# Optimization experiments

Measured on AMD Instinct MI355X. Metric: run time of the kernel, lower is better.

## Reference

```python
import jax, jax.numpy as jnp
import numpy as np

H = 16          # num_heads
R = 4           # query compression ratio
WIN = 128       # sliding window size
NEG = -1e9      # finite mask value (safe softmax grads)


def setup_inputs() -> dict:
    key = jax.random.key(0)
    k0, k1, k2, k3, k4 = jax.random.split(key, 5)
    B, S, D = 4, 4096, 2048
    inputs = jax.random.normal(k0, (B, S, D), jnp.float32)
    attention_mask = jnp.ones((B, S), jnp.int32)
    s = 0.02
    Wq = jax.random.normal(k1, (D, D), jnp.float32) * s
    Wk = jax.random.normal(k2, (D, D), jnp.float32) * s
    Wv = jax.random.normal(k3, (D, D), jnp.float32) * s
    Wo = jax.random.normal(k4, (D, D), jnp.float32) * s
    return {"inputs": inputs, "attention_mask": attention_mask,
            "Wq": Wq, "Wk": Wk, "Wv": Wv, "Wo": Wo}


def _forward(inputs, attention_mask, Wq, Wk, Wv, Wo):
    B, S, D = inputs.shape
    dh = D // H
    scale = 1.0 / np.sqrt(dh).astype(np.float32)
    Cs = (S + R - 1) // R            # compressed query length (S % R == 0 here)
    win = min(WIN, S)
    ws = max(0, S - win)             # window start

    # Q projection -> [B,H,S,dh] -> compress groups of R by mean -> [B,H,Cs,dh]
    q = jnp.einsum('bsd,od->bso', inputs, Wq)
    q = q.reshape(B, S, H, dh).transpose(0, 2, 1, 3)
    qc = q.reshape(B, H, Cs, R, dh).mean(axis=3)

    # K/V only over the recent window
    wx = inputs[:, ws:ws + win, :]
    k = jnp.einsum('bsd,od->bso', wx, Wk).reshape(B, win, H, dh).transpose(0, 2, 1, 3)
    v = jnp.einsum('bsd,od->bso', wx, Wv).reshape(B, win, H, dh).transpose(0, 2, 1, 3)

    scores = jnp.einsum('bhqd,bhkd->bhqk', qc, k) * scale

    # causal mask: each compressed query sits at position (i+1)*R-1
    qpos = (jnp.arange(Cs) + 1) * R - 1                     # [Cs]
    wpos = ws + jnp.arange(win)
    causal = wpos[None, :] <= qpos[:, None]
    qbw = qpos < ws                                         # queries fully before window
    causal = causal.at[:, 0].set(causal[:, 0] | qbw)
    pad_ok = (attention_mask[:, ws:ws + win] != 0)
    full = causal[None, None, :, :] & pad_ok[:, None, None, :]

    scores = jnp.where(full, scores, NEG)
    weights = jax.nn.softmax(scores, axis=-1)
    out = jnp.einsum('bhqk,bhkd->bhqd', weights, v)         # [B,H,Cs,dh]
    out = out.transpose(0, 2, 1, 3).reshape(B, Cs, D)
    out = jnp.einsum('bsd,od->bso', out, Wo)

    if Cs != S:  # linear interpolation back to seq_len (align_corners=False)
        out = jax.image.resize(out, (B, S, D), method='linear')
    return out


def reference(inputs, attention_mask, Wq, Wk, Wv, Wo):
    return _forward(inputs, attention_mask, Wq, Wk, Wv, Wo)
```

## Files before the change

### kernel.cpp

```cpp
#include <hip/hip_runtime.h>
#include <hip/hip_bf16.h>


typedef __attribute__((ext_vector_type(8))) short short8;
typedef __attribute__((ext_vector_type(4))) float f32x4;

#define QP_SLICE  (128 * 2048)
#define KV_SLICE  (512 * 2048)
#define YO_STRIDE (132 * 2048)

__device__ __forceinline__ unsigned short f2bf(float f){
  unsigned int x = __float_as_uint(f);
  return (unsigned short)((x + 0x7fffu + ((x >> 16) & 1u)) >> 16);
}
__device__ __forceinline__ float bf2f(unsigned short u){
  return __uint_as_float(((unsigned int)u) << 16);
}
__device__ __forceinline__ float bflo(unsigned int u){ return __uint_as_float(u << 16); }
__device__ __forceinline__ float bfhi(unsigned int u){ return __uint_as_float(u & 0xffff0000u); }
__device__ __forceinline__ unsigned int pk2(float lo, float hi){
  return ((unsigned int)f2bf(hi) << 16) | (unsigned int)f2bf(lo);
}
__device__ __forceinline__ short8 cvt8(float4 x, float4 y){
  union { unsigned int u[4]; short8 s; } r;
  r.u[0] = pk2(x.x, x.y); r.u[1] = pk2(x.z, x.w);
  r.u[2] = pk2(y.x, y.y); r.u[3] = pk2(y.z, y.w);
  return r.s;
}

__global__ __launch_bounds__(256) void prep_kernel(
    const float* __restrict__ inp,
    const float* __restrict__ Wq, const float* __restrict__ Wk,
    const float* __restrict__ Wv, const float* __restrict__ Wo,
    unsigned short* __restrict__ Wb,
    unsigned short* __restrict__ Awx, unsigned short* __restrict__ Aq)
{
  const int bx = blockIdx.x;
  if (bx < 8192){
    const int idx = bx * 256 + threadIdx.x;
    const int w = idx >> 19;
    const int sub = idx & 524287;
    const float* src = (w == 0) ? Wq : (w == 1) ? Wk : (w == 2) ? Wv : Wo;
    const float* p = src + (size_t)sub * 8;
    *(short8*)&Wb[(size_t)w * 4194304 + (size_t)sub * 8] =
        cvt8(*(const float4*)p, *(const float4*)(p + 4));
  } else if (bx < 8704){
    const int idx = (bx - 8192) * 256 + threadIdx.x;
    const int b = idx >> 15;
    const int j = (idx >> 8) & 127;
    const int d8 = (idx & 255) * 8;
    const float* p = inp + ((size_t)b * 4096 + 3968 + j) * 2048 + d8;
    *(short8*)&Awx[((size_t)b * 128 + j) * 2048 + d8] =
        cvt8(*(const float4*)p, *(const float4*)(p + 4));
  } else {
    const int idx = (bx - 8704) * 256 + threadIdx.x;
    const int b = idx >> 13;
    const int c = (idx >> 8) & 31;
    const int d8 = (idx & 255) * 8;
    const float* p = inp + ((size_t)b * 4096 + 3968 + 4 * c) * 2048 + d8;
    float4 x0 = *(const float4*)(p);
    float4 x1 = *(const float4*)(p + 2048);
    float4 x2 = *(const float4*)(p + 4096);
    float4 x3 = *(const float4*)(p + 6144);
    float4 y0 = *(const float4*)(p + 4);
    float4 y1 = *(const float4*)(p + 2052);
    float4 y2 = *(const float4*)(p + 4100);
    float4 y3 = *(const float4*)(p + 6148);
    float4 xm, ym;
    xm.x = 0.25f * (x0.x + x1.x + x2.x + x3.x);
    xm.y = 0.25f * (x0.y + x1.y + x2.y + x3.y);
    xm.z = 0.25f * (x0.z + x1.z + x2.z + x3.z);
    xm.w = 0.25f * (x0.w + x1.w + x2.w + x3.w);
    ym.x = 0.25f * (y0.x + y1.x + y2.x + y3.x);
    ym.y = 0.25f * (y0.y + y1.y + y2.y + y3.y);
    ym.z = 0.25f * (y0.z + y1.z + y2.z + y3.z);
    ym.w = 0.25f * (y0.w + y1.w + y2.w + y3.w);
    *(short8*)&Aq[((size_t)b * 32 + c) * 2048 + d8] = cvt8(xm, ym);
  }
}

__device__ __forceinline__ void stage_tile(
    const unsigned short* __restrict__ A, const unsigned short* __restrict__ W,
    int row0, int n0, int kt,
    unsigned short* As, unsigned short* Bs, int wid, int lane)
{
  const int r = lane >> 3, u = (lane & 7) * 8;
  #pragma unroll
  for (int i = 0; i < 4; ++i){
    const int c = wid * 4 + i;
    __builtin_amdgcn_global_load_lds(
        (const __attribute__((address_space(1))) void*)(A + (size_t)(row0 + c * 8 + r) * 2048 + kt + u),
        (__attribute__((address_space(3))) void*)(As + c * 512),
        16, 0, 0);
    __builtin_amdgcn_global_load_lds(
        (const __attribute__((address_space(1))) void*)(W + (size_t)(n0 + c * 8 + r) * 2048 + kt + u),
        (__attribute__((address_space(3))) void*)(Bs + c * 512),
        16, 0, 0);
  }
}

template<bool OUT_BF16>
__device__ __forceinline__ void gemm_body(
    const unsigned short* __restrict__ A, const unsigned short* __restrict__ W,
    unsigned short* __restrict__ Cb, float* __restrict__ Cf,
    int M, int row0, int n0, int kbase, int nsteps,
    unsigned short* L)
{
  const int tid  = threadIdx.x;
  const int lane = tid & 63;
  const int wid  = tid >> 6;
  const int wr = wid >> 1, wc = wid & 1;

  f32x4 acc[4][4] = {};

  stage_tile(A, W, row0, n0, kbase, L, L + 8192, wid, lane);
  int cur = 0;

  for (int t = 0; t < nsteps; ++t){
    __syncthreads();
    const int nxt = cur ^ 1;
    if (t + 1 < nsteps)
      stage_tile(A, W, row0, n0, kbase + (t + 1) * 64,
                 L + nxt * 16384, L + nxt * 16384 + 8192, wid, lane);
    const unsigned short* As = L + cur * 16384;
    const unsigned short* Bs = As + 8192;
    #pragma unroll
    for (int ks = 0; ks < 2; ++ks){
      short8 av[4], bv[4];
      #pragma unroll
      for (int f = 0; f < 4; ++f)
        av[f] = *(const short8*)&As[(wr * 64 + f * 16 + (lane & 15)) * 64 + ks * 32 + (lane >> 4) * 8];
      #pragma unroll
      for (int n = 0; n < 4; ++n)
        bv[n] = *(const short8*)&Bs[(wc * 64 + n * 16 + (lane & 15)) * 64 + ks * 32 + (lane >> 4) * 8];
      #pragma unroll
      for (int f = 0; f < 4; ++f)
        #pragma unroll
        for (int n = 0; n < 4; ++n)
          acc[f][n] = __builtin_amdgcn_mfma_f32_16x16x32_bf16(av[f], bv[n], acc[f][n], 0, 0, 0);
    }
    cur = nxt;
  }

  #pragma unroll
  for (int f = 0; f < 4; ++f){
    #pragma unroll
    for (int n = 0; n < 4; ++n){
      const int col = n0 + wc * 64 + n * 16 + (lane & 15);
      #pragma unroll
      for (int r = 0; r < 4; ++r){
        const int row = row0 + wr * 64 + f * 16 + (lane >> 4) * 4 + r;
        if (row < M){
          if (OUT_BF16) Cb[(size_t)row * 2048 + col] = f2bf(acc[f][n][r]);
          else          Cf[(size_t)row * 2048 + col] = acc[f][n][r];
        }
      }
    }
  }
}

__global__ __launch_bounds__(256, 2) void qkv_kernel(
    const unsigned short* __restrict__ Aq, const unsigned short* __restrict__ Awx,
    const unsigned short* __restrict__ Wb,
    unsigned short* __restrict__ Qp, unsigned short* __restrict__ Kp,
    unsigned short* __restrict__ Vp)
{
  __shared__ __align__(16) unsigned short L[4 * 16384 / 2];
  const int nt = blockIdx.x, gy = blockIdx.y;
  if (gy < 4){
    gemm_body<true>(Aq, Wb, Qp + gy * QP_SLICE, nullptr,
                    128, 0, nt * 128, gy * 512, 8, L);
  } else if (gy < 20){
    const int idx = gy - 4, mt = idx >> 2, ksp = idx & 3;
    gemm_body<true>(Awx, Wb + 4194304, Kp + ksp * KV_SLICE, nullptr,
                    512, mt * 128, nt * 128, ksp * 512, 8, L);
  } else {
    const int idx = gy - 20, mt = idx >> 2, ksp = idx & 3;
    gemm_body<true>(Awx, Wb + 8388608, Vp + ksp * KV_SLICE, nullptr,
                    512, mt * 128, nt * 128, ksp * 512, 8, L);
  }
}

__global__ __launch_bounds__(256, 2) void o_kernel(
    const unsigned short* __restrict__ Ao, const unsigned short* __restrict__ Wb,
    float* __restrict__ Yop)
{
  __shared__ __align__(16) unsigned short L[32768];
  gemm_body<false>(Ao, Wb + 12582912, nullptr, Yop + (size_t)blockIdx.z * YO_STRIDE,
                   132, blockIdx.y * 128, blockIdx.x * 128, blockIdx.z * 512, 8, L);
}

__global__ __launch_bounds__(256) void attn_kernel(
    const unsigned short* __restrict__ Qp, const unsigned short* __restrict__ Kp,
    const unsigned short* __restrict__ Vp, const int* __restrict__ amask,
    unsigned short* __restrict__ Ao)
{
  const int b = blockIdx.x >> 4;
  const int h = blockIdx.x & 15;
  __shared__ float Qs[32][129];
  __shared__ unsigned int Ks[128][65];
  __shared__ unsigned int Vs[128][65];
  __shared__ float Wt[32][132];
  __shared__ float msk[128];
  const int tid = threadIdx.x;

  for (int i = tid; i < 32 * 128; i += 256){
    int cq = i >> 7, d = i & 127;
    size_t off = (size_t)(b * 32 + cq) * 2048 + h * 128 + d;
    Qs[cq][d] = bf2f(Qp[off]) + bf2f(Qp[off + QP_SLICE]) +
                bf2f(Qp[off + 2 * QP_SLICE]) + bf2f(Qp[off + 3 * QP_SLICE]);
  }
  for (int i = tid; i < 128 * 64; i += 256){
    int j = i >> 6, du = i & 63;
    size_t off = (size_t)(b * 128 + j) * 2048 + h * 128 + du * 2;
    unsigned int k0 = *(const unsigned int*)(Kp + off);
    unsigned int k1 = *(const unsigned int*)(Kp + off + KV_SLICE);
    unsigned int k2 = *(const unsigned int*)(Kp + off + 2 * KV_SLICE);
    unsigned int k3 = *(const unsigned int*)(Kp + off + 3 * KV_SLICE);
    unsigned int v0 = *(const unsigned int*)(Vp + off);
    unsigned int v1 = *(const unsigned int*)(Vp + off + KV_SLICE);
    unsigned int v2 = *(const unsigned int*)(Vp + off + 2 * KV_SLICE);
    unsigned int v3 = *(const unsigned int*)(Vp + off + 3 * KV_SLICE);
    Ks[j][du] = pk2(bflo(k0) + bflo(k1) + bflo(k2) + bflo(k3),
                    bfhi(k0) + bfhi(k1) + bfhi(k2) + bfhi(k3));
    Vs[j][du] = pk2(bflo(v0) + bflo(v1) + bflo(v2) + bflo(v3),
                    bfhi(v0) + bfhi(v1) + bfhi(v2) + bfhi(v3));
  }
  if (tid < 128){
    msk[tid] = (amask[b * 4096 + 3968 + tid] != 0) ? 1.f : 0.f;
    size_t off = (size_t)(b * 128) * 2048 + h * 128 + tid;
    Ao[(size_t)(b * 33) * 2048 + h * 128 + tid] =
        f2bf(bf2f(Vp[off]) + bf2f(Vp[off + KV_SLICE]) +
             bf2f(Vp[off + 2 * KV_SLICE]) + bf2f(Vp[off + 3 * KV_SLICE]));
  }
  __syncthreads();

  const int cq = tid >> 3, jg = tid & 7;
  const int jmax = 4 * cq + 3;
  const float scale = 0.088388347648318447f;

  float s[16];
  {
    float sacc[16];
    #pragma unroll
    for (int jj = 0; jj < 16; ++jj) sacc[jj] = 0.f;
    for (int du = 0; du < 64; ++du){
      float q0 = Qs[cq][2 * du], q1 = Qs[cq][2 * du + 1];
      #pragma unroll
      for (int jj = 0; jj < 16; ++jj){
        unsigned int u = Ks[jg * 16 + jj][du];
        sacc[jj] += q0 * bflo(u) + q1 * bfhi(u);
      }
    }
    #pragma unroll
    for (int jj = 0; jj < 16; ++jj){
      int j = jg * 16 + jj;
      bool ok = (j <= jmax) && (msk[j] > 0.5f);
      s[jj] = ok ? sacc[jj] * scale : -1e9f;
    }
  }
  float m = s[0];
  #pragma unroll
  for (int jj = 1; jj < 16; ++jj) m = fmaxf(m, s[jj]);
  #pragma unroll
  for (int off = 1; off < 8; off <<= 1) m = fmaxf(m, __shfl_xor(m, off, 8));
  float sum = 0.f;
  #pragma unroll
  for (int jj = 0; jj < 16; ++jj){ s[jj] = expf(s[jj] - m); sum += s[jj]; }
  #pragma unroll
  for (int off = 1; off < 8; off <<= 1) sum += __shfl_xor(sum, off, 8);
  const float inv = 1.f / sum;
  #pragma unroll
  for (int jj = 0; jj < 16; ++jj) Wt[cq][jg * 16 + jj] = s[jj] * inv;
  __syncthreads();

  const int dg = tid & 7;
  float o[16];
  #pragma unroll
  for (int e = 0; e < 16; ++e) o[e] = 0.f;
  for (int j = 0; j < 128; ++j){
    float w = Wt[cq][j];
    #pragma unroll
    for (int du = 0; du < 8; ++du){
      unsigned int u = Vs[j][dg * 8 + du];
      o[2 * du]     += w * bflo(u);
      o[2 * du + 1] += w * bfhi(u);
    }
  }
  unsigned short* dst = Ao + (size_t)(b * 33 + 1 + cq) * 2048 + h * 128 + dg * 16;
  #pragma unroll
  for (int e = 0; e < 16; ++e) dst[e] = f2bf(o[e]);
}

__global__ __launch_bounds__(256) void resize_kernel(
    const float* __restrict__ Yop, float* __restrict__ out)
{
  const int rowid = blockIdx.x;
  const int b = rowid >> 12;
  const int i = rowid & 4095;
  float c  = i * 0.25f - 0.375f;
  float fl = floorf(c);
  int   j0 = (int)fl;
  float f  = c - fl;
  int   j1 = j0 + 1;
  j0 = max(0, min(j0, 1023));
  j1 = max(0, min(j1, 1023));
  const int ri0 = b * 33 + (j0 <= 991 ? 0 : j0 - 991);
  const int ri1 = b * 33 + (j1 <= 991 ? 0 : j1 - 991);
  const float* r0 = Yop + (size_t)ri0 * 2048;
  const float* r1 = Yop + (size_t)ri1 * 2048;
  float* op = out + (size_t)rowid * 2048;
  const int t = threadIdx.x;
  const bool same = (ri0 == ri1);
  #pragma unroll
  for (int q = 0; q < 2; ++q){
    int d = q * 1024 + t * 4;
    float4 a0 = *(const float4*)(r0 + d);
    float4 a1 = *(const float4*)(r0 + d + YO_STRIDE);
    float4 a2 = *(const float4*)(r0 + d + 2 * YO_STRIDE);
    float4 a3 = *(const float4*)(r0 + d + 3 * YO_STRIDE);
    float4 a;
    a.x = a0.x + a1.x + a2.x + a3.x;
    a.y = a0.y + a1.y + a2.y + a3.y;
    a.z = a0.z + a1.z + a2.z + a3.z;
    a.w = a0.w + a1.w + a2.w + a3.w;
    float4 o = a;
    if (!same){
      float4 b0 = *(const float4*)(r1 + d);
      float4 b1 = *(const float4*)(r1 + d + YO_STRIDE);
      float4 b2 = *(const float4*)(r1 + d + 2 * YO_STRIDE);
      float4 b3 = *(const float4*)(r1 + d + 3 * YO_STRIDE);
      float4 bb;
      bb.x = b0.x + b1.x + b2.x + b3.x;
      bb.y = b0.y + b1.y + b2.y + b3.y;
      bb.z = b0.z + b1.z + b2.z + b3.z;
      bb.w = b0.w + b1.w + b2.w + b3.w;
      o.x = a.x + f * (bb.x - a.x);
      o.y = a.y + f * (bb.y - a.y);
      o.z = a.z + f * (bb.z - a.z);
      o.w = a.w + f * (bb.w - a.w);
    }
    *(float4*)(op + d) = o;
  }
}

extern "C" void kernel_launch(void* const* d_in, const int* in_sizes, int n_in,
                              void* d_out, int out_size, void* d_ws, size_t ws_size,
                              hipStream_t stream)
{
  const float* inp   = (const float*)d_in[0];
  const int*   amask = (const int*)d_in[1];
  const float* Wq = (const float*)d_in[2];
  const float* Wk = (const float*)d_in[3];
  const float* Wv = (const float*)d_in[4];
  const float* Wo = (const float*)d_in[5];
  float* out = (float*)d_out;

  char* ws = (char*)d_ws;
  unsigned short* Wb  = (unsigned short*)(ws);
  unsigned short* Aq  = (unsigned short*)(ws + 33554432);
  unsigned short* Awx = (unsigned short*)(ws + 34078720);
  unsigned short* Qp  = (unsigned short*)(ws + 36175872);
  unsigned short* Kp  = (unsigned short*)(ws + 38273024);
  unsigned short* Vp  = (unsigned short*)(ws + 46661632);
  unsigned short* Ao  = (unsigned short*)(ws + 55050240);
  float*          Yop = (float*)(ws + 56623104);

  prep_kernel<<<8832, 256, 0, stream>>>(inp, Wq, Wk, Wv, Wo, Wb, Awx, Aq);
  qkv_kernel<<<dim3(16, 36), 256, 0, stream>>>(Aq, Awx, Wb, Qp, Kp, Vp);
  attn_kernel<<<64, 256, 0, stream>>>(Qp, Kp, Vp, amask, Ao);
  o_kernel<<<dim3(16, 2, 4), 256, 0, stream>>>(Ao, Wb, Yop);
  resize_kernel<<<16384, 256, 0, stream>>>(Yop, out);
}
```

Baseline: 118.1 us.

## Swizzle LDS tile layout and drop split-K in output projection

Applies an XOR swizzle to the 16-byte chunk index when staging A/W tiles into LDS and when reading MFMA fragments, to avoid LDS bank conflicts. The output projection now runs the full K=2048 reduction in one block instead of four split-K partials. This lets the resize kernel read one row pair instead of summing four partial buffers. The cost is fewer blocks (32 instead of 128) for the O GEMM, each doing a longer serial K loop, which reduces parallelism.

```diff
diff --git a/kernel.cpp b/kernel.cpp
--- a/kernel.cpp
+++ b/kernel.cpp
@@ -7,7 +7,6 @@
 
 #define QP_SLICE  (128 * 2048)
 #define KV_SLICE  (512 * 2048)
-#define YO_STRIDE (132 * 2048)
 
 __device__ __forceinline__ unsigned short f2bf(float f){
   unsigned int x = __float_as_uint(f);
@@ -84,16 +83,17 @@
     int row0, int n0, int kt,
     unsigned short* As, unsigned short* Bs, int wid, int lane)
 {
-  const int r = lane >> 3, u = (lane & 7) * 8;
+  const int r  = lane >> 3;
+  const int ug = ((lane & 7) ^ r) * 8;
   #pragma unroll
   for (int i = 0; i < 4; ++i){
     const int c = wid * 4 + i;
     __builtin_amdgcn_global_load_lds(
-        (const __attribute__((address_space(1))) void*)(A + (size_t)(row0 + c * 8 + r) * 2048 + kt + u),
+        (const __attribute__((address_space(1))) void*)(A + (size_t)(row0 + c * 8 + r) * 2048 + kt + ug),
         (__attribute__((address_space(3))) void*)(As + c * 512),
         16, 0, 0);
     __builtin_amdgcn_global_load_lds(
-        (const __attribute__((address_space(1))) void*)(W + (size_t)(n0 + c * 8 + r) * 2048 + kt + u),
+        (const __attribute__((address_space(1))) void*)(W + (size_t)(n0 + c * 8 + r) * 2048 + kt + ug),
         (__attribute__((address_space(3))) void*)(Bs + c * 512),
         16, 0, 0);
   }
@@ -127,12 +127,17 @@
     #pragma unroll
     for (int ks = 0; ks < 2; ++ks){
       short8 av[4], bv[4];
-      #pragma unroll
-      for (int f = 0; f < 4; ++f)
-        av[f] = *(const short8*)&As[(wr * 64 + f * 16 + (lane & 15)) * 64 + ks * 32 + (lane >> 4) * 8];
-      #pragma unroll
-      for (int n = 0; n < 4; ++n)
-        bv[n] = *(const short8*)&Bs[(wc * 64 + n * 16 + (lane & 15)) * 64 + ks * 32 + (lane >> 4) * 8];
+      const int unit = ks * 4 + (lane >> 4);
+      #pragma unroll
+      for (int f = 0; f < 4; ++f){
+        const int row = wr * 64 + f * 16 + (lane & 15);
+        av[f] = *(const short8*)&As[row * 64 + ((unit ^ (row & 7)) * 8)];
+      }
+      #pragma unroll
+      for (int n = 0; n < 4; ++n){
+        const int row = wc * 64 + n * 16 + (lane & 15);
+        bv[n] = *(const short8*)&Bs[row * 64 + ((unit ^ (row & 7)) * 8)];
+      }
       #pragma unroll
       for (int f = 0; f < 4; ++f)
         #pragma unroll
@@ -165,7 +170,7 @@
     unsigned short* __restrict__ Qp, unsigned short* __restrict__ Kp,
     unsigned short* __restrict__ Vp)
 {
-  __shared__ __align__(16) unsigned short L[4 * 16384 / 2];
+  __shared__ __align__(16) unsigned short L[32768];
   const int nt = blockIdx.x, gy = blockIdx.y;
   if (gy < 4){
     gemm_body<true>(Aq, Wb, Qp + gy * QP_SLICE, nullptr,
@@ -183,11 +188,11 @@
 
 __global__ __launch_bounds__(256, 2) void o_kernel(
     const unsigned short* __restrict__ Ao, const unsigned short* __restrict__ Wb,
-    float* __restrict__ Yop)
+    float* __restrict__ Yo)
 {
   __shared__ __align__(16) unsigned short L[32768];
-  gemm_body<false>(Ao, Wb + 12582912, nullptr, Yop + (size_t)blockIdx.z * YO_STRIDE,
-                   132, blockIdx.y * 128, blockIdx.x * 128, blockIdx.z * 512, 8, L);
+  gemm_body<false>(Ao, Wb + 12582912, nullptr, Yo,
+                   132, blockIdx.y * 128, blockIdx.x * 128, 0, 32, L);
 }
 
 __global__ __launch_bounds__(256) void attn_kernel(
@@ -293,7 +298,7 @@
 }
 
 __global__ __launch_bounds__(256) void resize_kernel(
-    const float* __restrict__ Yop, float* __restrict__ out)
+    const float* __restrict__ Yo, float* __restrict__ out)
 {
   const int rowid = blockIdx.x;
   const int b = rowid >> 12;
@@ -305,41 +310,20 @@
   int   j1 = j0 + 1;
   j0 = max(0, min(j0, 1023));
   j1 = max(0, min(j1, 1023));
-  const int ri0 = b * 33 + (j0 <= 991 ? 0 : j0 - 991);
-  const int ri1 = b * 33 + (j1 <= 991 ? 0 : j1 - 991);
-  const float* r0 = Yop + (size_t)ri0 * 2048;
-  const float* r1 = Yop + (size_t)ri1 * 2048;
+  const float* r0 = Yo + (size_t)(b * 33 + (j0 <= 991 ? 0 : j0 - 991)) * 2048;
+  const float* r1 = Yo + (size_t)(b * 33 + (j1 <= 991 ? 0 : j1 - 991)) * 2048;
   float* op = out + (size_t)rowid * 2048;
   const int t = threadIdx.x;
-  const bool same = (ri0 == ri1);
   #pragma unroll
   for (int q = 0; q < 2; ++q){
     int d = q * 1024 + t * 4;
-    float4 a0 = *(const float4*)(r0 + d);
-    float4 a1 = *(const float4*)(r0 + d + YO_STRIDE);
-    float4 a2 = *(const float4*)(r0 + d + 2 * YO_STRIDE);
-    float4 a3 = *(const float4*)(r0 + d + 3 * YO_STRIDE);
-    float4 a;
-    a.x = a0.x + a1.x + a2.x + a3.x;
-    a.y = a0.y + a1.y + a2.y + a3.y;
-    a.z = a0.z + a1.z + a2.z + a3.z;
-    a.w = a0.w + a1.w + a2.w + a3.w;
-    float4 o = a;
-    if (!same){
-      float4 b0 = *(const float4*)(r1 + d);
-      float4 b1 = *(const float4*)(r1 + d + YO_STRIDE);
-      float4 b2 = *(const float4*)(r1 + d + 2 * YO_STRIDE);
-      float4 b3 = *(const float4*)(r1 + d + 3 * YO_STRIDE);
-      float4 bb;
-      bb.x = b0.x + b1.x + b2.x + b3.x;
-      bb.y = b0.y + b1.y + b2.y + b3.y;
-      bb.z = b0.z + b1.z + b2.z + b3.z;
-      bb.w = b0.w + b1.w + b2.w + b3.w;
-      o.x = a.x + f * (bb.x - a.x);
-      o.y = a.y + f * (bb.y - a.y);
-      o.z = a.z + f * (bb.z - a.z);
-      o.w = a.w + f * (bb.w - a.w);
-    }
+    float4 a  = *(const float4*)(r0 + d);
+    float4 bb = *(const float4*)(r1 + d);
+    float4 o;
+    o.x = a.x + f * (bb.x - a.x);
+    o.y = a.y + f * (bb.y - a.y);
+    o.z = a.z + f * (bb.z - a.z);
+    o.w = a.w + f * (bb.w - a.w);
     *(float4*)(op + d) = o;
   }
 }
@@ -364,11 +348,11 @@
   unsigned short* Kp  = (unsigned short*)(ws + 38273024);
   unsigned short* Vp  = (unsigned short*)(ws + 46661632);
   unsigned short* Ao  = (unsigned short*)(ws + 55050240);
-  float*          Yop = (float*)(ws + 56623104);
+  float*          Yo  = (float*)(ws + 56098816);
 
   prep_kernel<<<8832, 256, 0, stream>>>(inp, Wq, Wk, Wv, Wo, Wb, Awx, Aq);
   qkv_kernel<<<dim3(16, 36), 256, 0, stream>>>(Aq, Awx, Wb, Qp, Kp, Vp);
   attn_kernel<<<64, 256, 0, stream>>>(Qp, Kp, Vp, amask, Ao);
-  o_kernel<<<dim3(16, 2, 4), 256, 0, stream>>>(Ao, Wb, Yop);
-  resize_kernel<<<16384, 256, 0, stream>>>(Yop, out);
-}
+  o_kernel<<<dim3(16, 2), 256, 0, stream>>>(Ao, Wb, Yo);
+  resize_kernel<<<16384, 256, 0, stream>>>(Yo, out);
+}
```

Result: slower. 122.5 us (+3.7%).

## Fuse fp32-to-bf16 weight conversion into GEMM loads and halve split-K

Applied to the files above, without the earlier changes.

Removes the separate prep pass that converted all four fp32 weight matrices and the window inputs to bf16. The GEMMs now read fp32 weights and window activations directly, converting them in registers before storing to a padded LDS tile. This replaces the async global-to-LDS double buffering with register prefetch and a 32-wide k step. Split-K drops from 4 to 2 partials, so attention and resize sum fewer slices. The trade is more fp32 traffic per GEMM tile, since weights are read at double width by every M-tile, and a less overlapped main loop.

```diff
diff --git a/kernel.cpp b/kernel.cpp
--- a/kernel.cpp
+++ b/kernel.cpp
@@ -5,6 +5,7 @@
 typedef __attribute__((ext_vector_type(8))) short short8;
 typedef __attribute__((ext_vector_type(4))) float f32x4;
 
+#define LDP 40
 #define QP_SLICE  (128 * 2048)
 #define KV_SLICE  (512 * 2048)
 #define YO_STRIDE (132 * 2048)
@@ -28,118 +29,116 @@
   return r.s;
 }
 
-__global__ __launch_bounds__(256) void prep_kernel(
-    const float* __restrict__ inp,
-    const float* __restrict__ Wq, const float* __restrict__ Wk,
-    const float* __restrict__ Wv, const float* __restrict__ Wo,
-    unsigned short* __restrict__ Wb,
-    unsigned short* __restrict__ Awx, unsigned short* __restrict__ Aq)
-{
-  const int bx = blockIdx.x;
-  if (bx < 8192){
-    const int idx = bx * 256 + threadIdx.x;
-    const int w = idx >> 19;
-    const int sub = idx & 524287;
-    const float* src = (w == 0) ? Wq : (w == 1) ? Wk : (w == 2) ? Wv : Wo;
-    const float* p = src + (size_t)sub * 8;
-    *(short8*)&Wb[(size_t)w * 4194304 + (size_t)sub * 8] =
-        cvt8(*(const float4*)p, *(const float4*)(p + 4));
-  } else if (bx < 8704){
-    const int idx = (bx - 8192) * 256 + threadIdx.x;
-    const int b = idx >> 15;
-    const int j = (idx >> 8) & 127;
-    const int d8 = (idx & 255) * 8;
-    const float* p = inp + ((size_t)b * 4096 + 3968 + j) * 2048 + d8;
-    *(short8*)&Awx[((size_t)b * 128 + j) * 2048 + d8] =
-        cvt8(*(const float4*)p, *(const float4*)(p + 4));
-  } else {
-    const int idx = (bx - 8704) * 256 + threadIdx.x;
-    const int b = idx >> 13;
-    const int c = (idx >> 8) & 31;
-    const int d8 = (idx & 255) * 8;
-    const float* p = inp + ((size_t)b * 4096 + 3968 + 4 * c) * 2048 + d8;
-    float4 x0 = *(const float4*)(p);
-    float4 x1 = *(const float4*)(p + 2048);
-    float4 x2 = *(const float4*)(p + 4096);
-    float4 x3 = *(const float4*)(p + 6144);
-    float4 y0 = *(const float4*)(p + 4);
-    float4 y1 = *(const float4*)(p + 2052);
-    float4 y2 = *(const float4*)(p + 4100);
-    float4 y3 = *(const float4*)(p + 6148);
-    float4 xm, ym;
-    xm.x = 0.25f * (x0.x + x1.x + x2.x + x3.x);
-    xm.y = 0.25f * (x0.y + x1.y + x2.y + x3.y);
-    xm.z = 0.25f * (x0.z + x1.z + x2.z + x3.z);
-    xm.w = 0.25f * (x0.w + x1.w + x2.w + x3.w);
-    ym.x = 0.25f * (y0.x + y1.x + y2.x + y3.x);
-    ym.y = 0.25f * (y0.y + y1.y + y2.y + y3.y);
-    ym.z = 0.25f * (y0.z + y1.z + y2.z + y3.z);
-    ym.w = 0.25f * (y0.w + y1.w + y2.w + y3.w);
-    *(short8*)&Aq[((size_t)b * 32 + c) * 2048 + d8] = cvt8(xm, ym);
-  }
-}
-
-__device__ __forceinline__ void stage_tile(
-    const unsigned short* __restrict__ A, const unsigned short* __restrict__ W,
-    int row0, int n0, int kt,
-    unsigned short* As, unsigned short* Bs, int wid, int lane)
-{
-  const int r = lane >> 3, u = (lane & 7) * 8;
-  #pragma unroll
-  for (int i = 0; i < 4; ++i){
-    const int c = wid * 4 + i;
-    __builtin_amdgcn_global_load_lds(
-        (const __attribute__((address_space(1))) void*)(A + (size_t)(row0 + c * 8 + r) * 2048 + kt + u),
-        (__attribute__((address_space(3))) void*)(As + c * 512),
-        16, 0, 0);
-    __builtin_amdgcn_global_load_lds(
-        (const __attribute__((address_space(1))) void*)(W + (size_t)(n0 + c * 8 + r) * 2048 + kt + u),
-        (__attribute__((address_space(3))) void*)(Bs + c * 512),
-        16, 0, 0);
-  }
-}
-
-template<bool OUT_BF16>
+__global__ __launch_bounds__(256) void prep_means(
+    const float* __restrict__ inp, unsigned short* __restrict__ Aq)
+{
+  const int idx = blockIdx.x * 256 + threadIdx.x;
+  const int b = idx >> 13;
+  const int c = (idx >> 8) & 31;
+  const int d8 = (idx & 255) * 8;
+  const float* p = inp + ((size_t)b * 4096 + 3968 + 4 * c) * 2048 + d8;
+  float4 x0 = *(const float4*)(p);
+  float4 x1 = *(const float4*)(p + 2048);
+  float4 x2 = *(const float4*)(p + 4096);
+  float4 x3 = *(const float4*)(p + 6144);
+  float4 y0 = *(const float4*)(p + 4);
+  float4 y1 = *(const float4*)(p + 2052);
+  float4 y2 = *(const float4*)(p + 4100);
+  float4 y3 = *(const float4*)(p + 6148);
+  float4 xm, ym;
+  xm.x = 0.25f * (x0.x + x1.x + x2.x + x3.x);
+  xm.y = 0.25f * (x0.y + x1.y + x2.y + x3.y);
+  xm.z = 0.25f * (x0.z + x1.z + x2.z + x3.z);
+  xm.w = 0.25f * (x0.w + x1.w + x2.w + x3.w);
+  ym.x = 0.25f * (y0.x + y1.x + y2.x + y3.x);
+  ym.y = 0.25f * (y0.y + y1.y + y2.y + y3.y);
+  ym.z = 0.25f * (y0.z + y1.z + y2.z + y3.z);
+  ym.w = 0.25f * (y0.w + y1.w + y2.w + y3.w);
+  *(short8*)&Aq[((size_t)b * 32 + c) * 2048 + d8] = cvt8(xm, ym);
+}
+
+template<int AMODE, bool OUT_BF16>
 __device__ __forceinline__ void gemm_body(
-    const unsigned short* __restrict__ A, const unsigned short* __restrict__ W,
+    const void* __restrict__ Abase, const float* __restrict__ W,
     unsigned short* __restrict__ Cb, float* __restrict__ Cf,
     int M, int row0, int n0, int kbase, int nsteps,
-    unsigned short* L)
+    unsigned short* As, unsigned short* Bs)
 {
   const int tid  = threadIdx.x;
   const int lane = tid & 63;
   const int wid  = tid >> 6;
   const int wr = wid >> 1, wc = wid & 1;
 
+  const int arow = tid >> 1;
+  const int h    = (tid & 1) * 16;
+
+  int ga = row0 + arow; if (ga > M - 1) ga = M - 1;
+  const float*          ArowF = nullptr;
+  const unsigned short* ArowB = nullptr;
+  if constexpr (AMODE == 1)
+    ArowF = (const float*)Abase + ((size_t)(ga >> 7) * 4096 + 3968 + (ga & 127)) * 2048;
+  else
+    ArowB = (const unsigned short*)Abase + (size_t)ga * 2048;
+  const float* Wrow = W + (size_t)(n0 + arow) * 2048;
+
   f32x4 acc[4][4] = {};
-
-  stage_tile(A, W, row0, n0, kbase, L, L + 8192, wid, lane);
-  int cur = 0;
+  short8 a0, a1, b0, b1;
+
+  {
+    const int kt = kbase;
+    if constexpr (AMODE == 1){
+      a0 = cvt8(*(const float4*)(ArowF + kt + h), *(const float4*)(ArowF + kt + h + 4));
+      a1 = cvt8(*(const float4*)(ArowF + kt + h + 8), *(const float4*)(ArowF + kt + h + 12));
+    } else {
+      a0 = *(const short8*)(ArowB + kt + h);
+      a1 = *(const short8*)(ArowB + kt + h + 8);
+    }
+    b0 = cvt8(*(const float4*)(Wrow + kt + h), *(const float4*)(Wrow + kt + h + 4));
+    b1 = cvt8(*(const float4*)(Wrow + kt + h + 8), *(const float4*)(Wrow + kt + h + 12));
+    *(short8*)&As[arow * LDP + h]     = a0;
+    *(short8*)&As[arow * LDP + h + 8] = a1;
+    *(short8*)&Bs[arow * LDP + h]     = b0;
+    *(short8*)&Bs[arow * LDP + h + 8] = b1;
+  }
+  __syncthreads();
 
   for (int t = 0; t < nsteps; ++t){
-    __syncthreads();
-    const int nxt = cur ^ 1;
-    if (t + 1 < nsteps)
-      stage_tile(A, W, row0, n0, kbase + (t + 1) * 64,
-                 L + nxt * 16384, L + nxt * 16384 + 8192, wid, lane);
-    const unsigned short* As = L + cur * 16384;
-    const unsigned short* Bs = As + 8192;
-    #pragma unroll
-    for (int ks = 0; ks < 2; ++ks){
+    const bool pf = (t + 1) < nsteps;
+    if (pf){
+      const int kt = kbase + (t + 1) * 32;
+      if constexpr (AMODE == 1){
+        a0 = cvt8(*(const float4*)(ArowF + kt + h), *(const float4*)(ArowF + kt + h + 4));
+        a1 = cvt8(*(const float4*)(ArowF + kt + h + 8), *(const float4*)(ArowF + kt + h + 12));
+      } else {
+        a0 = *(const short8*)(ArowB + kt + h);
+        a1 = *(const short8*)(ArowB + kt + h + 8);
+      }
+      b0 = cvt8(*(const float4*)(Wrow + kt + h), *(const float4*)(Wrow + kt + h + 4));
+      b1 = cvt8(*(const float4*)(Wrow + kt + h + 8), *(const float4*)(Wrow + kt + h + 12));
+    }
+    {
       short8 av[4], bv[4];
+      const int ko = (lane >> 4) * 8;
       #pragma unroll
       for (int f = 0; f < 4; ++f)
-        av[f] = *(const short8*)&As[(wr * 64 + f * 16 + (lane & 15)) * 64 + ks * 32 + (lane >> 4) * 8];
+        av[f] = *(const short8*)&As[(wr * 64 + f * 16 + (lane & 15)) * LDP + ko];
       #pragma unroll
       for (int n = 0; n < 4; ++n)
-        bv[n] = *(const short8*)&Bs[(wc * 64 + n * 16 + (lane & 15)) * 64 + ks * 32 + (lane >> 4) * 8];
+        bv[n] = *(const short8*)&Bs[(wc * 64 + n * 16 + (lane & 15)) * LDP + ko];
       #pragma unroll
       for (int f = 0; f < 4; ++f)
         #pragma unroll
         for (int n = 0; n < 4; ++n)
           acc[f][n] = __builtin_amdgcn_mfma_f32_16x16x32_bf16(av[f], bv[n], acc[f][n], 0, 0, 0);
     }
-    cur = nxt;
+    __syncthreads();
+    if (pf){
+      *(short8*)&As[arow * LDP + h]     = a0;
+      *(short8*)&As[arow * LDP + h + 8] = a1;
+      *(short8*)&Bs[arow * LDP + h]     = b0;
+      *(short8*)&Bs[arow * LDP + h + 8] = b1;
+      __syncthreads();
+    }
   }
 
   #pragma unroll
@@ -159,35 +158,36 @@
   }
 }
 
-__global__ __launch_bounds__(256, 2) void qkv_kernel(
-    const unsigned short* __restrict__ Aq, const unsigned short* __restrict__ Awx,
-    const unsigned short* __restrict__ Wb,
+__global__ __launch_bounds__(256, 4) void qkv_kernel(
+    const float* __restrict__ inp, const unsigned short* __restrict__ Aq,
+    const float* __restrict__ Wq, const float* __restrict__ Wk, const float* __restrict__ Wv,
     unsigned short* __restrict__ Qp, unsigned short* __restrict__ Kp,
     unsigned short* __restrict__ Vp)
 {
-  __shared__ __align__(16) unsigned short L[4 * 16384 / 2];
-  const int nt = blockIdx.x, gy = blockIdx.y;
-  if (gy < 4){
-    gemm_body<true>(Aq, Wb, Qp + gy * QP_SLICE, nullptr,
-                    128, 0, nt * 128, gy * 512, 8, L);
-  } else if (gy < 20){
-    const int idx = gy - 4, mt = idx >> 2, ksp = idx & 3;
-    gemm_body<true>(Awx, Wb + 4194304, Kp + ksp * KV_SLICE, nullptr,
-                    512, mt * 128, nt * 128, ksp * 512, 8, L);
+  __shared__ __align__(16) unsigned short As[128 * LDP];
+  __shared__ __align__(16) unsigned short Bs[128 * LDP];
+  const int nt = blockIdx.x, gy = blockIdx.y, ksp = blockIdx.z;
+  if (gy == 0){
+    gemm_body<0, true>(Aq, Wq, Qp + ksp * QP_SLICE, nullptr,
+                       128, 0, nt * 128, ksp * 1024, 32, As, Bs);
+  } else if (gy < 5){
+    gemm_body<1, true>(inp, Wk, Kp + ksp * KV_SLICE, nullptr,
+                       512, (gy - 1) * 128, nt * 128, ksp * 1024, 32, As, Bs);
   } else {
-    const int idx = gy - 20, mt = idx >> 2, ksp = idx & 3;
-    gemm_body<true>(Awx, Wb + 8388608, Vp + ksp * KV_SLICE, nullptr,
-                    512, mt * 128, nt * 128, ksp * 512, 8, L);
-  }
-}
-
-__global__ __launch_bounds__(256, 2) void o_kernel(
-    const unsigned short* __restrict__ Ao, const unsigned short* __restrict__ Wb,
+    gemm_body<1, true>(inp, Wv, Vp + ksp * KV_SLICE, nullptr,
+                       512, (gy - 5) * 128, nt * 128, ksp * 1024, 32, As, Bs);
+  }
+}
+
+__global__ __launch_bounds__(256, 4) void o_kernel(
+    const unsigned short* __restrict__ Ao, const float* __restrict__ Wo,
     float* __restrict__ Yop)
 {
-  __shared__ __align__(16) unsigned short L[32768];
-  gemm_body<false>(Ao, Wb + 12582912, nullptr, Yop + (size_t)blockIdx.z * YO_STRIDE,
-                   132, blockIdx.y * 128, blockIdx.x * 128, blockIdx.z * 512, 8, L);
+  __shared__ __align__(16) unsigned short As[128 * LDP];
+  __shared__ __align__(16) unsigned short Bs[128 * LDP];
+  gemm_body<0, false>(Ao, Wo, nullptr, Yop + (size_t)blockIdx.z * YO_STRIDE,
+                      132, blockIdx.y * 128, blockIdx.x * 128, blockIdx.z * 1024, 32,
+                      As, Bs);
 }
 
 __global__ __launch_bounds__(256) void attn_kernel(
@@ -207,31 +207,23 @@
   for (int i = tid; i < 32 * 128; i += 256){
     int cq = i >> 7, d = i & 127;
     size_t off = (size_t)(b * 32 + cq) * 2048 + h * 128 + d;
-    Qs[cq][d] = bf2f(Qp[off]) + bf2f(Qp[off + QP_SLICE]) +
-                bf2f(Qp[off + 2 * QP_SLICE]) + bf2f(Qp[off + 3 * QP_SLICE]);
+    Qs[cq][d] = bf2f(Qp[off]) + bf2f(Qp[off + QP_SLICE]);
   }
   for (int i = tid; i < 128 * 64; i += 256){
     int j = i >> 6, du = i & 63;
     size_t off = (size_t)(b * 128 + j) * 2048 + h * 128 + du * 2;
     unsigned int k0 = *(const unsigned int*)(Kp + off);
     unsigned int k1 = *(const unsigned int*)(Kp + off + KV_SLICE);
-    unsigned int k2 = *(const unsigned int*)(Kp + off + 2 * KV_SLICE);
-    unsigned int k3 = *(const unsigned int*)(Kp + off + 3 * KV_SLICE);
     unsigned int v0 = *(const unsigned int*)(Vp + off);
     unsigned int v1 = *(const unsigned int*)(Vp + off + KV_SLICE);
-    unsigned int v2 = *(const unsigned int*)(Vp + off + 2 * KV_SLICE);
-    unsigned int v3 = *(const unsigned int*)(Vp + off + 3 * KV_SLICE);
-    Ks[j][du] = pk2(bflo(k0) + bflo(k1) + bflo(k2) + bflo(k3),
-                    bfhi(k0) + bfhi(k1) + bfhi(k2) + bfhi(k3));
-    Vs[j][du] = pk2(bflo(v0) + bflo(v1) + bflo(v2) + bflo(v3),
-                    bfhi(v0) + bfhi(v1) + bfhi(v2) + bfhi(v3));
+    Ks[j][du] = pk2(bflo(k0) + bflo(k1), bfhi(k0) + bfhi(k1));
+    Vs[j][du] = pk2(bflo(v0) + bflo(v1), bfhi(v0) + bfhi(v1));
   }
   if (tid < 128){
     msk[tid] = (amask[b * 4096 + 3968 + tid] != 0) ? 1.f : 0.f;
     size_t off = (size_t)(b * 128) * 2048 + h * 128 + tid;
     Ao[(size_t)(b * 33) * 2048 + h * 128 + tid] =
-        f2bf(bf2f(Vp[off]) + bf2f(Vp[off + KV_SLICE]) +
-             bf2f(Vp[off + 2 * KV_SLICE]) + bf2f(Vp[off + 3 * KV_SLICE]));
+        f2bf(bf2f(Vp[off]) + bf2f(Vp[off + KV_SLICE]));
   }
   __syncthreads();
 
@@ -317,24 +309,14 @@
     int d = q * 1024 + t * 4;
     float4 a0 = *(const float4*)(r0 + d);
     float4 a1 = *(const float4*)(r0 + d + YO_STRIDE);
-    float4 a2 = *(const float4*)(r0 + d + 2 * YO_STRIDE);
-    float4 a3 = *(const float4*)(r0 + d + 3 * YO_STRIDE);
     float4 a;
-    a.x = a0.x + a1.x + a2.x + a3.x;
-    a.y = a0.y + a1.y + a2.y + a3.y;
-    a.z = a0.z + a1.z + a2.z + a3.z;
-    a.w = a0.w + a1.w + a2.w + a3.w;
+    a.x = a0.x + a1.x; a.y = a0.y + a1.y; a.z = a0.z + a1.z; a.w = a0.w + a1.w;
     float4 o = a;
     if (!same){
       float4 b0 = *(const float4*)(r1 + d);
       float4 b1 = *(const float4*)(r1 + d + YO_STRIDE);
-      float4 b2 = *(const float4*)(r1 + d + 2 * YO_STRIDE);
-      float4 b3 = *(const float4*)(r1 + d + 3 * YO_STRIDE);
       float4 bb;
-      bb.x = b0.x + b1.x + b2.x + b3.x;
-      bb.y = b0.y + b1.y + b2.y + b3.y;
-      bb.z = b0.z + b1.z + b2.z + b3.z;
-      bb.w = b0.w + b1.w + b2.w + b3.w;
+      bb.x = b0.x + b1.x; bb.y = b0.y + b1.y; bb.z = b0.z + b1.z; bb.w = b0.w + b1.w;
       o.x = a.x + f * (bb.x - a.x);
       o.y = a.y + f * (bb.y - a.y);
       o.z = a.z + f * (bb.z - a.z);
@@ -357,18 +339,16 @@
   float* out = (float*)d_out;
 
   char* ws = (char*)d_ws;
-  unsigned short* Wb  = (unsigned short*)(ws);
-  unsigned short* Aq  = (unsigned short*)(ws + 33554432);
-  unsigned short* Awx = (unsigned short*)(ws + 34078720);
-  unsigned short* Qp  = (unsigned short*)(ws + 36175872);
-  unsigned short* Kp  = (unsigned short*)(ws + 38273024);
-  unsigned short* Vp  = (unsigned short*)(ws + 46661632);
-  unsigned short* Ao  = (unsigned short*)(ws + 55050240);
-  float*          Yop = (float*)(ws + 56623104);
-
-  prep_kernel<<<8832, 256, 0, stream>>>(inp, Wq, Wk, Wv, Wo, Wb, Awx, Aq);
-  qkv_kernel<<<dim3(16, 36), 256, 0, stream>>>(Aq, Awx, Wb, Qp, Kp, Vp);
+  unsigned short* Aq  = (unsigned short*)(ws);
+  unsigned short* Qp  = (unsigned short*)(ws + 524288);
+  unsigned short* Kp  = (unsigned short*)(ws + 1572864);
+  unsigned short* Vp  = (unsigned short*)(ws + 5767168);
+  unsigned short* Ao  = (unsigned short*)(ws + 9961472);
+  float*          Yop = (float*)(ws + 10502144);
+
+  prep_means<<<128, 256, 0, stream>>>(inp, Aq);
+  qkv_kernel<<<dim3(16, 9, 2), 256, 0, stream>>>(inp, Aq, Wq, Wk, Wv, Qp, Kp, Vp);
   attn_kernel<<<64, 256, 0, stream>>>(Qp, Kp, Vp, amask, Ao);
-  o_kernel<<<dim3(16, 2, 4), 256, 0, stream>>>(Ao, Wb, Yop);
+  o_kernel<<<dim3(16, 2, 2), 256, 0, stream>>>(Ao, Wo, Yop);
   resize_kernel<<<16384, 256, 0, stream>>>(Yop, out);
 }
```

New measurement: 138.5 us. 1.17x slower.

## Swizzle LDS GEMM tiles and halve QKV split-K partials

Applied to the files above, without the earlier changes.

Applies an XOR swizzle to the 16-byte chunk index when staging A/W tiles into LDS and when reading MFMA fragments, which is meant to remove LDS bank conflicts on the fragment reads. Separately, it cuts the QKV GEMM split-K factor from 4 to 2, giving 16 k-steps per block and half as many blocks. This halves the partial-sum traffic that the attention kernel has to read and reduce. The trade-off is fewer blocks (288 instead of 576) and therefore less parallelism in the QKV projection.

```diff
diff --git a/kernel.cpp b/kernel.cpp
--- a/kernel.cpp
+++ b/kernel.cpp
@@ -84,16 +84,17 @@
     int row0, int n0, int kt,
     unsigned short* As, unsigned short* Bs, int wid, int lane)
 {
-  const int r = lane >> 3, u = (lane & 7) * 8;
+  const int r  = lane >> 3;
+  const int ug = ((lane & 7) ^ r) * 8;
   #pragma unroll
   for (int i = 0; i < 4; ++i){
     const int c = wid * 4 + i;
     __builtin_amdgcn_global_load_lds(
-        (const __attribute__((address_space(1))) void*)(A + (size_t)(row0 + c * 8 + r) * 2048 + kt + u),
+        (const __attribute__((address_space(1))) void*)(A + (size_t)(row0 + c * 8 + r) * 2048 + kt + ug),
         (__attribute__((address_space(3))) void*)(As + c * 512),
         16, 0, 0);
     __builtin_amdgcn_global_load_lds(
-        (const __attribute__((address_space(1))) void*)(W + (size_t)(n0 + c * 8 + r) * 2048 + kt + u),
+        (const __attribute__((address_space(1))) void*)(W + (size_t)(n0 + c * 8 + r) * 2048 + kt + ug),
         (__attribute__((address_space(3))) void*)(Bs + c * 512),
         16, 0, 0);
   }
@@ -127,12 +128,17 @@
     #pragma unroll
     for (int ks = 0; ks < 2; ++ks){
       short8 av[4], bv[4];
-      #pragma unroll
-      for (int f = 0; f < 4; ++f)
-        av[f] = *(const short8*)&As[(wr * 64 + f * 16 + (lane & 15)) * 64 + ks * 32 + (lane >> 4) * 8];
-      #pragma unroll
-      for (int n = 0; n < 4; ++n)
-        bv[n] = *(const short8*)&Bs[(wc * 64 + n * 16 + (lane & 15)) * 64 + ks * 32 + (lane >> 4) * 8];
+      const int unit = ks * 4 + (lane >> 4);
+      #pragma unroll
+      for (int f = 0; f < 4; ++f){
+        const int row = wr * 64 + f * 16 + (lane & 15);
+        av[f] = *(const short8*)&As[row * 64 + ((unit ^ (row & 7)) * 8)];
+      }
+      #pragma unroll
+      for (int n = 0; n < 4; ++n){
+        const int row = wc * 64 + n * 16 + (lane & 15);
+        bv[n] = *(const short8*)&Bs[row * 64 + ((unit ^ (row & 7)) * 8)];
+      }
       #pragma unroll
       for (int f = 0; f < 4; ++f)
         #pragma unroll
@@ -165,19 +171,19 @@
     unsigned short* __restrict__ Qp, unsigned short* __restrict__ Kp,
     unsigned short* __restrict__ Vp)
 {
-  __shared__ __align__(16) unsigned short L[4 * 16384 / 2];
+  __shared__ __align__(16) unsigned short L[32768];
   const int nt = blockIdx.x, gy = blockIdx.y;
-  if (gy < 4){
+  if (gy < 2){
     gemm_body<true>(Aq, Wb, Qp + gy * QP_SLICE, nullptr,
-                    128, 0, nt * 128, gy * 512, 8, L);
-  } else if (gy < 20){
-    const int idx = gy - 4, mt = idx >> 2, ksp = idx & 3;
+                    128, 0, nt * 128, gy * 1024, 16, L);
+  } else if (gy < 10){
+    const int idx = gy - 2, mt = idx >> 1, ksp = idx & 1;
     gemm_body<true>(Awx, Wb + 4194304, Kp + ksp * KV_SLICE, nullptr,
-                    512, mt * 128, nt * 128, ksp * 512, 8, L);
+                    512, mt * 128, nt * 128, ksp * 1024, 16, L);
   } else {
-    const int idx = gy - 20, mt = idx >> 2, ksp = idx & 3;
+    const int idx = gy - 10, mt = idx >> 1, ksp = idx & 1;
     gemm_body<true>(Awx, Wb + 8388608, Vp + ksp * KV_SLICE, nullptr,
-                    512, mt * 128, nt * 128, ksp * 512, 8, L);
+                    512, mt * 128, nt * 128, ksp * 1024, 16, L);
   }
 }
 
@@ -207,31 +213,23 @@
   for (int i = tid; i < 32 * 128; i += 256){
     int cq = i >> 7, d = i & 127;
     size_t off = (size_t)(b * 32 + cq) * 2048 + h * 128 + d;
-    Qs[cq][d] = bf2f(Qp[off]) + bf2f(Qp[off + QP_SLICE]) +
-                bf2f(Qp[off + 2 * QP_SLICE]) + bf2f(Qp[off + 3 * QP_SLICE]);
+    Qs[cq][d] = bf2f(Qp[off]) + bf2f(Qp[off + QP_SLICE]);
   }
   for (int i = tid; i < 128 * 64; i += 256){
     int j = i >> 6, du = i & 63;
     size_t off = (size_t)(b * 128 + j) * 2048 + h * 128 + du * 2;
     unsigned int k0 = *(const unsigned int*)(Kp + off);
     unsigned int k1 = *(const unsigned int*)(Kp + off + KV_SLICE);
-    unsigned int k2 = *(const unsigned int*)(Kp + off + 2 * KV_SLICE);
-    unsigned int k3 = *(const unsigned int*)(Kp + off + 3 * KV_SLICE);
     unsigned int v0 = *(const unsigned int*)(Vp + off);
     unsigned int v1 = *(const unsigned int*)(Vp + off + KV_SLICE);
-    unsigned int v2 = *(const unsigned int*)(Vp + off + 2 * KV_SLICE);
-    unsigned int v3 = *(const unsigned int*)(Vp + off + 3 * KV_SLICE);
-    Ks[j][du] = pk2(bflo(k0) + bflo(k1) + bflo(k2) + bflo(k3),
-                    bfhi(k0) + bfhi(k1) + bfhi(k2) + bfhi(k3));
-    Vs[j][du] = pk2(bflo(v0) + bflo(v1) + bflo(v2) + bflo(v3),
-                    bfhi(v0) + bfhi(v1) + bfhi(v2) + bfhi(v3));
+    Ks[j][du] = pk2(bflo(k0) + bflo(k1), bfhi(k0) + bfhi(k1));
+    Vs[j][du] = pk2(bflo(v0) + bflo(v1), bfhi(v0) + bfhi(v1));
   }
   if (tid < 128){
     msk[tid] = (amask[b * 4096 + 3968 + tid] != 0) ? 1.f : 0.f;
     size_t off = (size_t)(b * 128) * 2048 + h * 128 + tid;
     Ao[(size_t)(b * 33) * 2048 + h * 128 + tid] =
-        f2bf(bf2f(Vp[off]) + bf2f(Vp[off + KV_SLICE]) +
-             bf2f(Vp[off + 2 * KV_SLICE]) + bf2f(Vp[off + 3 * KV_SLICE]));
+        f2bf(bf2f(Vp[off]) + bf2f(Vp[off + KV_SLICE]));
   }
   __syncthreads();
 
@@ -361,13 +359,13 @@
   unsigned short* Aq  = (unsigned short*)(ws + 33554432);
   unsigned short* Awx = (unsigned short*)(ws + 34078720);
   unsigned short* Qp  = (unsigned short*)(ws + 36175872);
-  unsigned short* Kp  = (unsigned short*)(ws + 38273024);
-  unsigned short* Vp  = (unsigned short*)(ws + 46661632);
-  unsigned short* Ao  = (unsigned short*)(ws + 55050240);
-  float*          Yop = (float*)(ws + 56623104);
+  unsigned short* Kp  = (unsigned short*)(ws + 37224448);
+  unsigned short* Vp  = (unsigned short*)(ws + 41418752);
+  unsigned short* Ao  = (unsigned short*)(ws + 45613056);
+  float*          Yop = (float*)(ws + 46661632);
 
   prep_kernel<<<8832, 256, 0, stream>>>(inp, Wq, Wk, Wv, Wo, Wb, Awx, Aq);
-  qkv_kernel<<<dim3(16, 36), 256, 0, stream>>>(Aq, Awx, Wb, Qp, Kp, Vp);
+  qkv_kernel<<<dim3(16, 18), 256, 0, stream>>>(Aq, Awx, Wb, Qp, Kp, Vp);
   attn_kernel<<<64, 256, 0, stream>>>(Qp, Kp, Vp, amask, Ao);
   o_kernel<<<dim3(16, 2, 4), 256, 0, stream>>>(Ao, Wb, Yop);
   resize_kernel<<<16384, 256, 0, stream>>>(Yop, out);
```

New measurement: 111.3 us, median of 2. 5.8% less time.
